# Kernel optimization log

Measured on AMD Instinct MI355X. Metric: run time of the kernel, lower is better.

Reference implementation:

```python
import jax, jax.numpy as jnp
import numpy as np

C = 512
GROUPS = 32
EPS = 1e-6


def group_norm(x, w, b):
    # x: [B, C, H, W]
    B, Cc, H, W = x.shape
    xg = x.reshape(B, GROUPS, Cc // GROUPS, H, W)
    mean = xg.mean(axis=(2, 3, 4), keepdims=True)
    var = xg.var(axis=(2, 3, 4), keepdims=True)
    xg = (xg - mean) * jax.lax.rsqrt(var + EPS)
    x = xg.reshape(B, Cc, H, W)
    return x * w[None, :, None, None] + b[None, :, None, None]


def conv1x1(x, w, b):
    # 1x1 conv == per-pixel channel matmul; w: [Cout, Cin]
    return jnp.einsum('bchw,oc->bohw', x, w) + b[None, :, None, None]


def setup_inputs() -> dict:
    key = jax.random.key(0)
    ks = jax.random.split(key, 11)
    s = 1.0 / np.sqrt(C)
    d = {
        'x': jax.random.normal(ks[0], (2, C, 64, 64), dtype=jnp.float32),
        'gn_w': jnp.ones((C,), jnp.float32),
        'gn_b': jnp.zeros((C,), jnp.float32),
        'wq': jax.random.normal(ks[1], (C, C), jnp.float32) * s,
        'bq': jax.random.normal(ks[2], (C,), jnp.float32) * 0.01,
        'wk': jax.random.normal(ks[3], (C, C), jnp.float32) * s,
        'bk': jax.random.normal(ks[4], (C,), jnp.float32) * 0.01,
        'wv': jax.random.normal(ks[5], (C, C), jnp.float32) * s,
        'bv': jax.random.normal(ks[6], (C,), jnp.float32) * 0.01,
        'wo': jax.random.normal(ks[7], (C, C), jnp.float32) * s,
        'bo': jax.random.normal(ks[8], (C,), jnp.float32) * 0.01,
    }
    return d


def reference(x, gn_w, gn_b, wq, bq, wk, bk, wv, bv, wo, bo):
    B, Cc, H, W = x.shape
    h = group_norm(x, gn_w, gn_b)
    q = conv1x1(h, wq, bq)  # [B,C,H,W]
    k = conv1x1(h, wk, bk)
    v = conv1x1(h, wv, bv)
    N = H * W
    q = q.reshape(B, Cc, N).transpose(0, 2, 1)   # b n c
    k = k.reshape(B, Cc, N)                      # b c n
    v = v.reshape(B, Cc, N)                      # b c n
    attn = jnp.einsum('bic,bcj->bij', q, k) * (Cc ** -0.5)  # [B,N,N]
    attn = jax.nn.softmax(attn, axis=-1)
    # h_[b,c,i] = sum_j v[b,c,j] * attn[b,i,j]
    h_ = jnp.einsum('bcj,bij->bci', v, attn).reshape(B, Cc, H, W)
    h_ = conv1x1(h_, wo, bo)
    return x + h_
```

## Files before the change

kernel.cpp:

```cpp
#include <hip/hip_runtime.h>


typedef __attribute__((ext_vector_type(8))) short bf16x8;
typedef __attribute__((ext_vector_type(4))) float f32x4;
typedef unsigned short u16;
typedef unsigned int u32;

__device__ __forceinline__ u16 f2bf(float f) {
  u32 u = __builtin_bit_cast(u32, f);
  return (u16)((u + 0x7FFFu + ((u >> 16) & 1u)) >> 16);
}
__device__ __forceinline__ float bf2f(u16 u) {
  return __builtin_bit_cast(float, (u32)u << 16);
}
__device__ __forceinline__ void gll16(const void* g, void* l) {
  __builtin_amdgcn_global_load_lds((const __attribute__((address_space(1))) u32*)g,
                                   (__attribute__((address_space(3))) u32*)l, 16, 0, 0);
}

__global__ void zero_stats(float* __restrict__ stats) {
  if (threadIdx.x < 128) stats[threadIdx.x] = 0.f;
}

__global__ __launch_bounds__(256) void gn_stats(const float* __restrict__ x,
                                                float* __restrict__ stats) {
  int bg = blockIdx.x >> 3, slice = blockIdx.x & 7;
  const float4* xp = (const float4*)(x + (size_t)bg * 65536 + slice * 8192);
  int t = threadIdx.x;
  float s = 0.f, ss = 0.f;
  for (int i = t; i < 2048; i += 256) {
    float4 v = xp[i];
    s += v.x + v.y + v.z + v.w;
    ss += v.x * v.x + v.y * v.y + v.z * v.z + v.w * v.w;
  }
  for (int off = 32; off > 0; off >>= 1) {
    s += __shfl_down(s, off);
    ss += __shfl_down(ss, off);
  }
  __shared__ float rs[4], rss[4];
  if ((t & 63) == 0) { rs[t >> 6] = s; rss[t >> 6] = ss; }
  __syncthreads();
  if (t == 0) {
    atomicAdd(&stats[bg * 2 + 0], rs[0] + rs[1] + rs[2] + rs[3]);
    atomicAdd(&stats[bg * 2 + 1], rss[0] + rss[1] + rss[2] + rss[3]);
  }
}

__global__ __launch_bounds__(256) void gn_apply(
    const float* __restrict__ x, const float* __restrict__ w,
    const float* __restrict__ b, const float* __restrict__ stats,
    u16* __restrict__ ht) {
  int bg = blockIdx.x >> 3, slice = blockIdx.x & 7;
  int batch = bg >> 5, g = bg & 31;
  const float* xp = x + (size_t)bg * 65536;
  float mean = stats[bg * 2 + 0] * (1.f / 65536.f);
  float var = stats[bg * 2 + 1] * (1.f / 65536.f) - mean * mean;
  float rstd = rsqrtf(var + 1e-6f);
  float wsc[16], bsc[16];
#pragma unroll
  for (int cc = 0; cc < 16; ++cc) {
    float wv = w[g * 16 + cc];
    wsc[cc] = wv * rstd;
    bsc[cc] = b[g * 16 + cc] - mean * wsc[cc];
  }
  u16* hp = ht + (size_t)batch * 4096 * 512 + g * 16;
  int t = threadIdx.x;
  for (int n = slice * 512 + t; n < slice * 512 + 512; n += 256) {
    union { u16 pk[16]; uint4 v4[2]; } u;
#pragma unroll
    for (int cc = 0; cc < 16; ++cc)
      u.pk[cc] = f2bf(xp[cc * 4096 + n] * wsc[cc] + bsc[cc]);
    uint4* dst = (uint4*)(hp + (size_t)n * 512);
    dst[0] = u.v4[0];
    dst[1] = u.v4[1];
  }
}

__global__ __launch_bounds__(256) void wcvt_kernel(
    const float* __restrict__ wq, const float* __restrict__ wk,
    const float* __restrict__ wv, const float* __restrict__ wo,
    const float* __restrict__ bq, const float* __restrict__ bk,
    u16* __restrict__ Wqk, u16* __restrict__ Wv, u16* __restrict__ Wo,
    float* __restrict__ Bqk) {
  int i = blockIdx.x * 256 + threadIdx.x;
  Wqk[i] = f2bf(wq[i]);
  Wqk[262144 + i] = f2bf(wk[i]);
  Wv[i] = f2bf(wv[i]);
  Wo[i] = f2bf(wo[i]);
  if (i < 512) { Bqk[i] = bq[i]; Bqk[512 + i] = bk[i]; }
}

template <int BM, int BN, int MODE>
__global__ __launch_bounds__(256) void mfma_gemm(
    const u16* __restrict__ A, int sA, const u16* __restrict__ B, int sB,
    int K, const float* __restrict__ bias, const float* __restrict__ res,
    void* __restrict__ out, int ostr, float scale,
    u16* __restrict__ p1, u16* __restrict__ p2, u16* __restrict__ p3) {
  constexpr int TM = BM / 32, TN = BN / 32;
  constexpr int SIA = BM / 32, SIB = BN / 32;
  __shared__ char sm[(BM + BN) * 128];
  char* As = sm;
  char* Bs = sm + BM * 128;
  int t = threadIdx.x;
  int w = t >> 6, lane = t & 63, quad = lane >> 4, ln = lane & 15;
  int wm = w >> 1, wn = w & 1;
  int m0 = blockIdx.y * BM, n0 = blockIdx.x * BN;
  int kbase = (MODE == 5) ? blockIdx.z * K : 0;
  f32x4 acc[TM][TN] = {};

  for (int k0 = 0; k0 < K; k0 += 64) {
#pragma unroll
    for (int si = 0; si < SIA; ++si) {
      int s = (w * SIA + si) * 64 + lane;
      gll16(A + (size_t)(m0 + (s & (BM - 1))) * sA + kbase + k0 + (s / BM) * 8,
            As + (w * SIA + si) * 1024);
    }
#pragma unroll
    for (int si = 0; si < SIB; ++si) {
      int s = (w * SIB + si) * 64 + lane;
      gll16(B + (size_t)(n0 + (s & (BN - 1))) * sB + kbase + k0 + (s / BN) * 8,
            Bs + (w * SIB + si) * 1024);
    }
    __syncthreads();
#pragma unroll
    for (int ks = 0; ks < 2; ++ks) {
      bf16x8 af[TM], bfr[TN];
#pragma unroll
      for (int tm = 0; tm < TM; ++tm)
        af[tm] = *(const bf16x8*)(As + (((ks * 4 + quad) * BM) + wm * (BM / 2) + tm * 16 + ln) * 16);
#pragma unroll
      for (int tn = 0; tn < TN; ++tn)
        bfr[tn] = *(const bf16x8*)(Bs + (((ks * 4 + quad) * BN) + wn * (BN / 2) + tn * 16 + ln) * 16);
#pragma unroll
      for (int tm = 0; tm < TM; ++tm)
#pragma unroll
        for (int tn = 0; tn < TN; ++tn)
          acc[tm][tn] = __builtin_amdgcn_mfma_f32_16x16x32_bf16(af[tm], bfr[tn], acc[tm][tn], 0, 0, 0);
    }
    __syncthreads();
  }

  u16* pdst = nullptr;
  if (MODE == 5)
    pdst = (blockIdx.z == 0) ? (u16*)out : (blockIdx.z == 1) ? p1
         : (blockIdx.z == 2) ? p2 : p3;

#pragma unroll
  for (int tm = 0; tm < TM; ++tm) {
    int mb = m0 + wm * (BM / 2) + tm * 16 + quad * 4;
#pragma unroll
    for (int tn = 0; tn < TN; ++tn) {
      int n = n0 + wn * (BN / 2) + tn * 16 + ln;
      float bn = (MODE == 0) ? bias[n] : 0.f;
#pragma unroll
      for (int r = 0; r < 4; ++r) {
        int m = mb + r;
        float v = acc[tm][tn][r];
        if (MODE == 0) {
          ((u16*)out)[(size_t)m * ostr + n] = f2bf(v + bn);
        } else if (MODE == 1) {
          ((u16*)out)[(size_t)m * ostr + n] = f2bf(v + bias[m]);
        } else if (MODE == 2) {
          int bb = n >> 12, nn = n & 4095;
          size_t off = ((size_t)(bb * 512 + m)) * 4096 + nn;
          ((float*)out)[off] = v + bias[m] + res[off];
        } else if (MODE == 3) {
          ((u16*)out)[(size_t)m * ostr + n] = f2bf(v * scale);
        } else if (MODE == 4) {
          ((u16*)out)[(size_t)m * ostr + n] = f2bf(v);
        } else {
          pdst[(size_t)m * ostr + n] = f2bf(v);
        }
      }
    }
  }
}

__global__ __launch_bounds__(256) void softmax_kernel(u16* __restrict__ S) {
  u16* sp = S + (size_t)blockIdx.x * 4096;
  int t = threadIdx.x;
  int w = t >> 6;
  uint4 a = ((const uint4*)sp)[t * 2];
  uint4 b = ((const uint4*)sp)[t * 2 + 1];
  u32 words[8] = {a.x, a.y, a.z, a.w, b.x, b.y, b.z, b.w};
  float v[16];
#pragma unroll
  for (int i = 0; i < 8; ++i) {
    v[2 * i] = bf2f((u16)(words[i] & 0xFFFF));
    v[2 * i + 1] = bf2f((u16)(words[i] >> 16));
  }
  float mx = v[0];
#pragma unroll
  for (int i = 1; i < 16; ++i) mx = fmaxf(mx, v[i]);
#pragma unroll
  for (int d = 1; d < 64; d <<= 1) mx = fmaxf(mx, __shfl_xor(mx, d));
  __shared__ float red[8];
  if ((t & 63) == 0) red[w] = mx;
  __syncthreads();
  mx = fmaxf(fmaxf(red[0], red[1]), fmaxf(red[2], red[3]));
  float sum = 0.f;
#pragma unroll
  for (int i = 0; i < 16; ++i) {
    v[i] = __expf(v[i] - mx);
    sum += v[i];
  }
#pragma unroll
  for (int d = 1; d < 64; d <<= 1) sum += __shfl_xor(sum, d);
  if ((t & 63) == 0) red[4 + w] = sum;
  __syncthreads();
  float inv = 1.f / (red[4] + red[5] + red[6] + red[7]);
#pragma unroll
  for (int i = 0; i < 8; ++i)
    words[i] = (u32)f2bf(v[2 * i] * inv) | ((u32)f2bf(v[2 * i + 1] * inv) << 16);
  ((uint4*)sp)[t * 2] = make_uint4(words[0], words[1], words[2], words[3]);
  ((uint4*)sp)[t * 2 + 1] = make_uint4(words[4], words[5], words[6], words[7]);
}

__global__ __launch_bounds__(256) void combine4_kernel(
    u16* __restrict__ P0, const u16* __restrict__ P1,
    const u16* __restrict__ P2, const u16* __restrict__ P3) {
  int i = blockIdx.x * 256 + threadIdx.x;
  uint4 a = ((const uint4*)P0)[i];
  uint4 b = ((const uint4*)P1)[i];
  uint4 c = ((const uint4*)P2)[i];
  uint4 d = ((const uint4*)P3)[i];
  u32 wa[4] = {a.x, a.y, a.z, a.w}, wb[4] = {b.x, b.y, b.z, b.w};
  u32 wc[4] = {c.x, c.y, c.z, c.w}, wd[4] = {d.x, d.y, d.z, d.w};
  u32 wo_[4];
#pragma unroll
  for (int q = 0; q < 4; ++q) {
    float lo = bf2f((u16)(wa[q] & 0xFFFF)) + bf2f((u16)(wb[q] & 0xFFFF)) +
               bf2f((u16)(wc[q] & 0xFFFF)) + bf2f((u16)(wd[q] & 0xFFFF));
    float hi = bf2f((u16)(wa[q] >> 16)) + bf2f((u16)(wb[q] >> 16)) +
               bf2f((u16)(wc[q] >> 16)) + bf2f((u16)(wd[q] >> 16));
    wo_[q] = (u32)f2bf(lo) | ((u32)f2bf(hi) << 16);
  }
  ((uint4*)P0)[i] = make_uint4(wo_[0], wo_[1], wo_[2], wo_[3]);
}

extern "C" void kernel_launch(void* const* d_in, const int* in_sizes, int n_in,
                              void* d_out, int out_size, void* d_ws, size_t ws_size,
                              hipStream_t stream) {
  (void)in_sizes; (void)n_in; (void)out_size; (void)ws_size;
  const float* x = (const float*)d_in[0];
  const float* gnw = (const float*)d_in[1];
  const float* gnb = (const float*)d_in[2];
  const float* wq = (const float*)d_in[3];
  const float* bq = (const float*)d_in[4];
  const float* wk = (const float*)d_in[5];
  const float* bk = (const float*)d_in[6];
  const float* wv = (const float*)d_in[7];
  const float* bv = (const float*)d_in[8];
  const float* wo = (const float*)d_in[9];
  const float* bo = (const float*)d_in[10];
  float* out = (float*)d_out;

  char* ws = (char*)d_ws;
  u16* ht  = (u16*)(ws);
  u16* AOt = (u16*)(ws);
  u16* QKt = (u16*)(ws + 8388608);
  u16* S   = (u16*)(ws + 25165824);
  u16* Wqk = (u16*)(ws + 58720256);
  u16* Wv  = (u16*)(ws + 59768832);
  u16* Wo  = (u16*)(ws + 60293120);
  float* stats = (float*)(ws + 60817408);
  float* Bqk   = (float*)(ws + 60817920);
  u16* Vg  = (u16*)d_out;
  u16* P1g = (u16*)((char*)d_out + 8388608);
  u16* P2g = (u16*)((char*)d_out + 12582912);

  wcvt_kernel<<<1024, 256, 0, stream>>>(wq, wk, wv, wo, bq, bk, Wqk, Wv, Wo, Bqk);
  zero_stats<<<1, 128, 0, stream>>>(stats);
  gn_stats<<<512, 256, 0, stream>>>(x, stats);
  gn_apply<<<512, 256, 0, stream>>>(x, gnw, gnb, stats, ht);
  mfma_gemm<128, 128, 0><<<dim3(8, 64), 256, 0, stream>>>(
      ht, 512, Wqk, 512, 512, Bqk, nullptr, QKt, 1024, 1.f,
      nullptr, nullptr, nullptr);
  mfma_gemm<64, 128, 1><<<dim3(64, 8), 256, 0, stream>>>(
      Wv, 512, ht, 512, 512, bv, nullptr, Vg, 8192, 1.f,
      nullptr, nullptr, nullptr);
  for (int b = 0; b < 2; ++b) {
    const u16* Qb = QKt + (size_t)b * 4096 * 1024;
    mfma_gemm<128, 128, 3><<<dim3(32, 32), 256, 0, stream>>>(
        Qb, 1024, Qb + 512, 1024, 512, nullptr, nullptr, S, 4096,
        0.044194173824159216f, nullptr, nullptr, nullptr);
    softmax_kernel<<<4096, 256, 0, stream>>>(S);
    u16* P0 = AOt + (size_t)b * 4096 * 512;
    u16* P3 = QKt + (size_t)b * 4096 * 1024;
    mfma_gemm<128, 128, 5><<<dim3(4, 32, 4), 256, 0, stream>>>(
        S, 4096, Vg + (size_t)b * 4096, 8192, 1024, nullptr, nullptr,
        P0, 512, 1.f, P1g, P2g, P3);
    combine4_kernel<<<1024, 256, 0, stream>>>(P0, P1g, P2g, P3);
  }
  mfma_gemm<64, 128, 2><<<dim3(64, 8), 256, 0, stream>>>(
      Wo, 512, AOt, 512, 512, bo, x, out, 0, 1.f,
      nullptr, nullptr, nullptr);
}
```

Before: 373.3 us.

## Batch attention GEMMs and softmax across both images in single launches

```diff
diff --git a/kernel.cpp b/kernel.cpp
--- a/kernel.cpp
+++ b/kernel.cpp
@@ -16,10 +16,6 @@
 __device__ __forceinline__ void gll16(const void* g, void* l) {
   __builtin_amdgcn_global_load_lds((const __attribute__((address_space(1))) u32*)g,
                                    (__attribute__((address_space(3))) u32*)l, 16, 0, 0);
-}
-
-__global__ void zero_stats(float* __restrict__ stats) {
-  if (threadIdx.x < 128) stats[threadIdx.x] = 0.f;
 }
 
 __global__ __launch_bounds__(256) void gn_stats(const float* __restrict__ x,
@@ -81,13 +77,14 @@
     const float* __restrict__ wv, const float* __restrict__ wo,
     const float* __restrict__ bq, const float* __restrict__ bk,
     u16* __restrict__ Wqk, u16* __restrict__ Wv, u16* __restrict__ Wo,
-    float* __restrict__ Bqk) {
+    float* __restrict__ Bqk, float* __restrict__ stats) {
   int i = blockIdx.x * 256 + threadIdx.x;
   Wqk[i] = f2bf(wq[i]);
   Wqk[262144 + i] = f2bf(wk[i]);
   Wv[i] = f2bf(wv[i]);
   Wo[i] = f2bf(wo[i]);
   if (i < 512) { Bqk[i] = bq[i]; Bqk[512 + i] = bk[i]; }
+  if (blockIdx.x == 0 && threadIdx.x < 128) stats[threadIdx.x] = 0.f;
 }
 
 template <int BM, int BN, int MODE>
@@ -95,7 +92,8 @@
     const u16* __restrict__ A, int sA, const u16* __restrict__ B, int sB,
     int K, const float* __restrict__ bias, const float* __restrict__ res,
     void* __restrict__ out, int ostr, float scale,
-    u16* __restrict__ p1, u16* __restrict__ p2, u16* __restrict__ p3) {
+    u16* __restrict__ p1, u16* __restrict__ p2, u16* __restrict__ p3,
+    size_t zsA, size_t zsB, size_t zsO) {
   constexpr int TM = BM / 32, TN = BN / 32;
   constexpr int SIA = BM / 32, SIB = BN / 32;
   __shared__ char sm[(BM + BN) * 128];
@@ -105,20 +103,25 @@
   int w = t >> 6, lane = t & 63, quad = lane >> 4, ln = lane & 15;
   int wm = w >> 1, wn = w & 1;
   int m0 = blockIdx.y * BM, n0 = blockIdx.x * BN;
-  int kbase = (MODE == 5) ? blockIdx.z * K : 0;
+  int zb, ksplit;
+  if (MODE == 5) { zb = blockIdx.z >> 2; ksplit = blockIdx.z & 3; }
+  else           { zb = blockIdx.z;      ksplit = 0; }
+  const u16* Ab = A + (size_t)zb * zsA;
+  const u16* Bb = B + (size_t)zb * zsB;
+  int kbase = ksplit * K;
   f32x4 acc[TM][TN] = {};
 
   for (int k0 = 0; k0 < K; k0 += 64) {
 #pragma unroll
     for (int si = 0; si < SIA; ++si) {
       int s = (w * SIA + si) * 64 + lane;
-      gll16(A + (size_t)(m0 + (s & (BM - 1))) * sA + kbase + k0 + (s / BM) * 8,
+      gll16(Ab + (size_t)(m0 + (s & (BM - 1))) * sA + kbase + k0 + (s / BM) * 8,
             As + (w * SIA + si) * 1024);
     }
 #pragma unroll
     for (int si = 0; si < SIB; ++si) {
       int s = (w * SIB + si) * 64 + lane;
-      gll16(B + (size_t)(n0 + (s & (BN - 1))) * sB + kbase + k0 + (s / BN) * 8,
+      gll16(Bb + (size_t)(n0 + (s & (BN - 1))) * sB + kbase + k0 + (s / BN) * 8,
             Bs + (w * SIB + si) * 1024);
     }
     __syncthreads();
@@ -141,9 +144,13 @@
   }
 
   u16* pdst = nullptr;
-  if (MODE == 5)
-    pdst = (blockIdx.z == 0) ? (u16*)out : (blockIdx.z == 1) ? p1
-         : (blockIdx.z == 2) ? p2 : p3;
+  if (MODE == 5) {
+    pdst = (ksplit == 0) ? (u16*)out : (ksplit == 1) ? p1
+         : (ksplit == 2) ? p2 : p3;
+    pdst += (size_t)zb * zsO;
+  } else if (MODE != 2) {
+    pdst = (u16*)out + (size_t)zb * zsO;
+  }
 
 #pragma unroll
   for (int tm = 0; tm < TM; ++tm) {
@@ -157,17 +164,15 @@
         int m = mb + r;
         float v = acc[tm][tn][r];
         if (MODE == 0) {
-          ((u16*)out)[(size_t)m * ostr + n] = f2bf(v + bn);
+          pdst[(size_t)m * ostr + n] = f2bf(v + bn);
         } else if (MODE == 1) {
-          ((u16*)out)[(size_t)m * ostr + n] = f2bf(v + bias[m]);
+          pdst[(size_t)m * ostr + n] = f2bf(v + bias[m]);
         } else if (MODE == 2) {
           int bb = n >> 12, nn = n & 4095;
           size_t off = ((size_t)(bb * 512 + m)) * 4096 + nn;
           ((float*)out)[off] = v + bias[m] + res[off];
         } else if (MODE == 3) {
-          ((u16*)out)[(size_t)m * ostr + n] = f2bf(v * scale);
-        } else if (MODE == 4) {
-          ((u16*)out)[(size_t)m * ostr + n] = f2bf(v);
+          pdst[(size_t)m * ostr + n] = f2bf(v * scale);
         } else {
           pdst[(size_t)m * ostr + n] = f2bf(v);
         }
@@ -241,7 +246,7 @@
 extern "C" void kernel_launch(void* const* d_in, const int* in_sizes, int n_in,
                               void* d_out, int out_size, void* d_ws, size_t ws_size,
                               hipStream_t stream) {
-  (void)in_sizes; (void)n_in; (void)out_size; (void)ws_size;
+  (void)in_sizes; (void)n_in; (void)out_size;
   const float* x = (const float*)d_in[0];
   const float* gnw = (const float*)d_in[1];
   const float* gnb = (const float*)d_in[2];
@@ -255,44 +260,59 @@
   const float* bo = (const float*)d_in[10];
   float* out = (float*)d_out;
 
+  const bool BIG = ws_size >= (size_t)96 * 1024 * 1024;
   char* ws = (char*)d_ws;
   u16* ht  = (u16*)(ws);
   u16* AOt = (u16*)(ws);
   u16* QKt = (u16*)(ws + 8388608);
   u16* S   = (u16*)(ws + 25165824);
-  u16* Wqk = (u16*)(ws + 58720256);
-  u16* Wv  = (u16*)(ws + 59768832);
-  u16* Wo  = (u16*)(ws + 60293120);
-  float* stats = (float*)(ws + 60817408);
-  float* Bqk   = (float*)(ws + 60817920);
+  size_t woff = BIG ? 92274688u : 58720256u;
+  u16* Wqk = (u16*)(ws + woff);
+  u16* Wv  = (u16*)(ws + woff + 1048576);
+  u16* Wo  = (u16*)(ws + woff + 1572864);
+  float* stats = (float*)(ws + woff + 2097152);
+  float* Bqk   = (float*)(ws + woff + 2097664);
   u16* Vg  = (u16*)d_out;
   u16* P1g = (u16*)((char*)d_out + 8388608);
-  u16* P2g = (u16*)((char*)d_out + 12582912);
-
-  wcvt_kernel<<<1024, 256, 0, stream>>>(wq, wk, wv, wo, bq, bk, Wqk, Wv, Wo, Bqk);
-  zero_stats<<<1, 128, 0, stream>>>(stats);
+
+  wcvt_kernel<<<1024, 256, 0, stream>>>(wq, wk, wv, wo, bq, bk, Wqk, Wv, Wo,
+                                        Bqk, stats);
   gn_stats<<<512, 256, 0, stream>>>(x, stats);
   gn_apply<<<512, 256, 0, stream>>>(x, gnw, gnb, stats, ht);
   mfma_gemm<128, 128, 0><<<dim3(8, 64), 256, 0, stream>>>(
       ht, 512, Wqk, 512, 512, Bqk, nullptr, QKt, 1024, 1.f,
-      nullptr, nullptr, nullptr);
+      nullptr, nullptr, nullptr, 0, 0, 0);
   mfma_gemm<64, 128, 1><<<dim3(64, 8), 256, 0, stream>>>(
       Wv, 512, ht, 512, 512, bv, nullptr, Vg, 8192, 1.f,
-      nullptr, nullptr, nullptr);
-  for (int b = 0; b < 2; ++b) {
-    const u16* Qb = QKt + (size_t)b * 4096 * 1024;
-    mfma_gemm<128, 128, 3><<<dim3(32, 32), 256, 0, stream>>>(
-        Qb, 1024, Qb + 512, 1024, 512, nullptr, nullptr, S, 4096,
-        0.044194173824159216f, nullptr, nullptr, nullptr);
-    softmax_kernel<<<4096, 256, 0, stream>>>(S);
-    u16* P0 = AOt + (size_t)b * 4096 * 512;
-    u16* P3 = QKt + (size_t)b * 4096 * 1024;
-    mfma_gemm<128, 128, 5><<<dim3(4, 32, 4), 256, 0, stream>>>(
-        S, 4096, Vg + (size_t)b * 4096, 8192, 1024, nullptr, nullptr,
-        P0, 512, 1.f, P1g, P2g, P3);
-    combine4_kernel<<<1024, 256, 0, stream>>>(P0, P1g, P2g, P3);
+      nullptr, nullptr, nullptr, 0, 0, 0);
+
+  if (BIG) {
+    mfma_gemm<128, 128, 3><<<dim3(32, 32, 2), 256, 0, stream>>>(
+        QKt, 1024, QKt + 512, 1024, 512, nullptr, nullptr, S, 4096,
+        0.044194173824159216f, nullptr, nullptr, nullptr,
+        4194304u, 4194304u, 16777216u);
+    softmax_kernel<<<8192, 256, 0, stream>>>(S);
+    mfma_gemm<128, 128, 5><<<dim3(4, 32, 8), 256, 0, stream>>>(
+        S, 4096, Vg, 8192, 1024, nullptr, nullptr,
+        AOt, 512, 1.f, P1g, QKt, QKt + 4194304, 16777216u, 4096u, 2097152u);
+    combine4_kernel<<<2048, 256, 0, stream>>>(AOt, P1g, QKt, QKt + 4194304);
+  } else {
+    u16* P2g = (u16*)((char*)d_out + 12582912);
+    for (int b = 0; b < 2; ++b) {
+      const u16* Qb = QKt + (size_t)b * 4194304;
+      mfma_gemm<128, 128, 3><<<dim3(32, 32), 256, 0, stream>>>(
+          Qb, 1024, Qb + 512, 1024, 512, nullptr, nullptr, S, 4096,
+          0.044194173824159216f, nullptr, nullptr, nullptr, 0, 0, 0);
+      softmax_kernel<<<4096, 256, 0, stream>>>(S);
+      u16* P0 = AOt + (size_t)b * 2097152;
+      u16* P3 = QKt + (size_t)b * 4194304;
+      mfma_gemm<128, 128, 5><<<dim3(4, 32, 4), 256, 0, stream>>>(
+          S, 4096, Vg + (size_t)b * 4096, 8192, 1024, nullptr, nullptr,
+          P0, 512, 1.f, P1g, P2g, P3, 0, 0, 0);
+      combine4_kernel<<<1024, 256, 0, stream>>>(P0, P1g, P2g, P3);
+    }
   }
   mfma_gemm<64, 128, 2><<<dim3(64, 8), 256, 0, stream>>>(
       Wo, 512, AOt, 512, 512, bo, x, out, 0, 1.f,
-      nullptr, nullptr, nullptr);
-}
+      nullptr, nullptr, nullptr, 0, 0, 0);
+}
```

Result: faster. 364.8 us (-2.3%).
